# Kernel tuning notes

Hardware: AMD Instinct MI355X
Metric: run time of the kernel (lower is better)

## Reference

```python
import jax, jax.numpy as jnp
import numpy as np

B = 1024      # batch
DIN = 103     # generator/encoder input dim
L1, L2 = 64, 32   # encoder layer widths (latent = 32)
E = 8         # NUM_EXPERTS
GH = 64       # gating hidden width
H = 256       # generator hidden width
DOUT = 51     # generator output dim
EPS = 1e-5    # BatchNorm eps


def setup_inputs() -> dict:
    key = jax.random.key(0)
    ks = jax.random.split(key, 24)
    s = 0.05
    f32 = jnp.float32
    return {
        "x": jax.random.normal(ks[0], (B, DIN), f32),
        # encoder Linear + BN params
        "w1": jax.random.normal(ks[1], (L1, DIN), f32) * s,
        "b1": jnp.zeros((L1,), f32),
        "gamma1": jnp.ones((L1,), f32),
        "beta1": jnp.zeros((L1,), f32),
        "w2": jax.random.normal(ks[2], (L2, L1), f32) * s,
        "b2": jnp.zeros((L2,), f32),
        "gamma2": jnp.ones((L2,), f32),
        "beta2": jnp.zeros((L2,), f32),
        # gating MLP (latent 32 -> GH -> GH -> E, ELU, softmax)
        "gw1": jax.random.normal(ks[3], (GH, L2), f32) * s,
        "gb1": jnp.zeros((GH,), f32),
        "gw2": jax.random.normal(ks[4], (GH, GH), f32) * s,
        "gb2": jnp.zeros((GH,), f32),
        "gw3": jax.random.normal(ks[5], (E, GH), f32) * s,
        "gb3": jnp.zeros((E,), f32),
        # expert weight banks for 3-layer generator (MANN style)
        "ew1": jax.random.normal(ks[6], (E, DIN, H), f32) * s,
        "eb1": jnp.zeros((E, H), f32),
        "ew2": jax.random.normal(ks[7], (E, H, H), f32) * s,
        "eb2": jnp.zeros((E, H), f32),
        "ew3": jax.random.normal(ks[8], (E, H, DOUT), f32) * s,
        "eb3": jnp.zeros((E, DOUT), f32),
    }


def _batchnorm(h, gamma, beta):
    # training-mode BatchNorm1d: per-batch mean/var (biased var, matching torch)
    m = jnp.mean(h, axis=0)
    v = jnp.mean((h - m) ** 2, axis=0)
    return gamma * (h - m) * jax.lax.rsqrt(v + EPS) + beta


def reference(x, w1, b1, gamma1, beta1, w2, b2, gamma2, beta2,
              gw1, gb1, gw2, gb2, gw3, gb3,
              ew1, eb1, ew2, eb2, ew3, eb3):
    # in-place scale of last 3 features (x[:,100:103] *= 100)
    xs = x.at[:, 100:103].multiply(100.0)
    # encoder: Linear -> BN -> ReLU, twice
    h = jax.nn.relu(_batchnorm(xs @ w1.T + b1, gamma1, beta1))
    latent = jax.nn.relu(_batchnorm(h @ w2.T + b2, gamma2, beta2))
    # gating network -> blending coefficients BC [B, E]
    g = jax.nn.elu(latent @ gw1.T + gb1)
    g = jax.nn.elu(g @ gw2.T + gb2)
    bc = jax.nn.softmax(g @ gw3.T + gb3, axis=-1)
    # MANN-style generator: per-sample expert-blended weights
    wb1 = jnp.einsum('be,eih->bih', bc, ew1)   # [B, DIN, H]
    h1 = jax.nn.elu(jnp.einsum('bi,bih->bh', xs, wb1) + bc @ eb1)
    wb2 = jnp.einsum('be,ehk->bhk', bc, ew2)   # [B, H, H]
    h2 = jax.nn.elu(jnp.einsum('bh,bhk->bk', h1, wb2) + bc @ eb2)
    wb3 = jnp.einsum('be,eho->bho', bc, ew3)   # [B, H, DOUT]
    out = jnp.einsum('bh,bho->bo', h2, wb3) + bc @ eb3
    return out
```

## Files before the change

kernel.cpp:

```cpp
#include <hip/hip_runtime.h>
#include <math.h>


#define DIN 103
#define NE  8
#define HH  256
#define DOUT 51
#define EPSBN 1e-5f

typedef __attribute__((ext_vector_type(8))) short bf16x8;
typedef __attribute__((ext_vector_type(4))) float f32x4;
typedef __attribute__((ext_vector_type(8))) unsigned short us8;
typedef unsigned short ushort_t;

__device__ __forceinline__ float eluf(float v) { return v > 0.f ? v : (expf(v) - 1.f); }
__device__ __forceinline__ unsigned short bf16h(float f) {
  unsigned u = __float_as_uint(f);
  u += 0x7FFFu + ((u >> 16) & 1u);
  return (unsigned short)(u >> 16);
}
__device__ __forceinline__ float bf16f(unsigned short h) { return __uint_as_float(((unsigned)h) << 16); }
__device__ __forceinline__ void split_bf16(float v, unsigned short& h, unsigned short& l) {
  h = bf16h(v);
  l = bf16h(v - bf16f(h));
}
#define MFMA __builtin_amdgcn_mfma_f32_16x16x32_bf16

#define O_SLOTS1 0
#define O_SLOTS2 8192
#define O_BCG    12288
#define O_H1RAW  20480
#define O_H2RAW  86016
#define O_XSH    118784
#define O_XSL    184320
#define O_E1H    258048
#define O_E1L    389120
#define O_E2H    520192
#define O_E3H    782336
#define O_A1H    847872
#define O_A1L    978944
#define O_A2H    1110016
#define O_A2L    1241088

__global__ __launch_bounds__(256) void k_prep_enc1(
    const float* __restrict__ x, const float* __restrict__ w1, const float* __restrict__ b1,
    const float* __restrict__ ew1, const float* __restrict__ ew2, const float* __restrict__ ew3,
    float* __restrict__ ws) {
  __shared__ union {
    float tile[32][65];
    float xt[16][104];
    struct { float w1L[64 * DIN]; float xr[16][104]; float hb[16][64]; } e1;
  } sm;
  int bk = blockIdx.x, t = threadIdx.x;
  int l2 = t & 63, c = l2 & 15, q = l2 >> 4;

  if (bk < 256) {
    int nh = bk & 3, kc = (bk >> 2) & 7, e = bk >> 5;
    int k0 = kc * 32, n0 = nh * 64;
#pragma unroll
    for (int i = 0; i < 8; ++i) {
      int kl = (t >> 6) + i * 4;
      sm.tile[kl][t & 63] = ew2[((size_t)e * HH + k0 + kl) * HH + n0 + (t & 63)];
    }
    __syncthreads();
    int nsl = t >> 6;
    us8 H8;
#pragma unroll
    for (int j = 0; j < 8; ++j) H8[j] = bf16h(sm.tile[q * 8 + j][nsl * 16 + c]);
    size_t dst = (((size_t)(e * 16 + nh * 4 + nsl)) * 8 + kc) * 512 + l2 * 8;
    *(us8*)((ushort_t*)(ws + O_E2H) + dst) = H8;
  } else if (bk < 384) {
    int b2 = bk - 256;
    int nh = b2 & 3, kc = (b2 >> 2) & 3, e = b2 >> 4;
    int k0 = kc * 32, n0 = nh * 64;
#pragma unroll
    for (int i = 0; i < 8; ++i) {
      int kl = (t >> 6) + i * 4;
      int k = k0 + kl;
      sm.tile[kl][t & 63] = (k < DIN) ? ew1[((size_t)e * DIN + k) * HH + n0 + (t & 63)] : 0.f;
    }
    __syncthreads();
    int nsl = t >> 6;
    us8 H8, L8;
#pragma unroll
    for (int j = 0; j < 8; ++j) {
      unsigned short h, lo; split_bf16(sm.tile[q * 8 + j][nsl * 16 + c], h, lo);
      H8[j] = h; L8[j] = lo;
    }
    size_t dst = (((size_t)(e * 16 + nh * 4 + nsl)) * 4 + kc) * 512 + l2 * 8;
    *(us8*)((ushort_t*)(ws + O_E1H) + dst) = H8;
    *(us8*)((ushort_t*)(ws + O_E1L) + dst) = L8;
  } else if (bk < 448) {
    int b2 = bk - 384;
    int kc = b2 & 7, e = b2 >> 3;
    int k0 = kc * 32;
#pragma unroll
    for (int i = 0; i < 8; ++i) {
      int kl = (t >> 6) + i * 4;
      int n = t & 63;
      sm.tile[kl][n] = (n < DOUT) ? ew3[((size_t)e * HH + k0 + kl) * DOUT + n] : 0.f;
    }
    __syncthreads();
    int nsl = t >> 6;
    us8 H8;
#pragma unroll
    for (int j = 0; j < 8; ++j) H8[j] = bf16h(sm.tile[q * 8 + j][nsl * 16 + c]);
    size_t dst = (((size_t)(e * 4 + nsl)) * 8 + kc) * 512 + l2 * 8;
    *(us8*)((ushort_t*)(ws + O_E3H) + dst) = H8;
  } else if (bk < 512) {
    int msub = bk - 448;
    for (int i = t; i < 16 * 104; i += 256) {
      int b = i / 104, k = i - b * 104;
      float v = 0.f;
      if (k < DIN) { v = x[(size_t)(msub * 16 + b) * DIN + k]; if (k >= 100) v *= 100.f; }
      sm.xt[b][k] = v;
    }
    __syncthreads();
    int kc = t >> 6;
    int m = c;
    us8 H8, L8;
#pragma unroll
    for (int j = 0; j < 8; ++j) {
      int k = kc * 32 + q * 8 + j;
      float v = (k < 104) ? sm.xt[m][k] : 0.f;
      unsigned short h, lo; split_bf16(v, h, lo);
      H8[j] = h; L8[j] = lo;
    }
    size_t dst = ((size_t)msub * 4 + kc) * 512 + l2 * 8;
    *(us8*)((ushort_t*)(ws + O_XSH) + dst) = H8;
    *(us8*)((ushort_t*)(ws + O_XSL) + dst) = L8;
  } else {
    float* slots1 = ws + O_SLOTS1;
    float* h1raw  = ws + O_H1RAW;
    int bkl = bk - 512;
    int r0 = bkl * 16;
    for (int i = t; i < 64 * DIN; i += 256) sm.e1.w1L[i] = w1[i];
    for (int i = t; i < 16 * 104; i += 256) {
      int r = i / 104, c2 = i - r * 104;
      float v = 0.f;
      if (c2 < DIN) { v = x[(size_t)(r0 + r) * DIN + c2]; if (c2 >= 100) v *= 100.f; }
      sm.e1.xr[r][c2] = v;
    }
    __syncthreads();
#pragma unroll
    for (int i = 0; i < 4; ++i) {
      int idx = t + i * 256;
      int r = idx >> 6, j = idx & 63;
      float acc = b1[j];
      for (int k = 0; k < DIN; ++k) acc = fmaf(sm.e1.xr[r][k], sm.e1.w1L[j * DIN + k], acc);
      sm.e1.hb[r][j] = acc;
      h1raw[(size_t)(r0 + r) * 64 + j] = acc;
    }
    __syncthreads();
    if (t < 64) {
      float s = 0.f, qq = 0.f;
      for (int r = 0; r < 16; ++r) { float v = sm.e1.hb[r][t]; s += v; qq += v * v; }
      slots1[bkl * 128 + t] = s;
      slots1[bkl * 128 + 64 + t] = qq;
    }
  }
}

__global__ __launch_bounds__(256) void k_enc2(
    const float* __restrict__ gamma1, const float* __restrict__ beta1,
    const float* __restrict__ w2, const float* __restrict__ b2, float* __restrict__ ws) {
  __shared__ float w2T[64 * 33];
  __shared__ float red[128];
  __shared__ float sc1[64], sh1[64];
  __shared__ float h1b[16][64];
  __shared__ float hb2[16][32];
  float* slots1 = ws + O_SLOTS1;
  float* slots2 = ws + O_SLOTS2;
  float* h1raw  = ws + O_H1RAW;
  float* h2raw  = ws + O_H2RAW;
  int bk = blockIdx.x, t = threadIdx.x;
  int R0 = bk * 16;
  for (int i = t; i < 2048; i += 256) { int j = i >> 6, k = i & 63; w2T[k * 33 + j] = w2[i]; }
  if (t < 128) {
    float s = 0.f;
    for (int b = 0; b < 64; ++b) s += slots1[b * 128 + t];
    red[t] = s;
  }
  __syncthreads();
  if (t < 64) {
    float m = red[t] * (1.f / 1024.f);
    float v = red[64 + t] * (1.f / 1024.f) - m * m;
    float sc = gamma1[t] * rsqrtf(v + EPSBN);
    sc1[t] = sc; sh1[t] = beta1[t] - m * sc;
  }
  __syncthreads();
#pragma unroll
  for (int i = 0; i < 4; ++i) {
    int idx = t + i * 256;
    int r = idx >> 6, k = idx & 63;
    h1b[r][k] = fmaxf(fmaf(h1raw[(size_t)(R0 + r) * 64 + k], sc1[k], sh1[k]), 0.f);
  }
  __syncthreads();
#pragma unroll
  for (int i = 0; i < 2; ++i) {
    int o = t + i * 256;
    int r = o >> 5, j = o & 31;
    float acc = b2[j];
    for (int k = 0; k < 64; ++k) acc = fmaf(h1b[r][k], w2T[k * 33 + j], acc);
    hb2[r][j] = acc;
    h2raw[(size_t)(R0 + r) * 32 + j] = acc;
  }
  __syncthreads();
  if (t < 32) {
    float s = 0.f, q = 0.f;
    for (int r = 0; r < 16; ++r) { float v = hb2[r][t]; s += v; q += v * v; }
    slots2[bk * 64 + t] = s;
    slots2[bk * 64 + 32 + t] = q;
  }
}

__global__ __launch_bounds__(256) void k_gen1(
    const float* __restrict__ gamma2, const float* __restrict__ beta2,
    const float* __restrict__ gw1, const float* __restrict__ gb1,
    const float* __restrict__ gw2, const float* __restrict__ gb2,
    const float* __restrict__ gw3, const float* __restrict__ gb3,
    const float* __restrict__ eb1, float* __restrict__ ws) {
  __shared__ union {
    struct {
      float gw1L[64 * 33];
      float gw2L[64 * 65];
      float gw3L[8 * 65];
      float gb1L[64], gb2L[64], gb3L[8];
      float red2[64], sc2[32], sh2[32];
      float lat[16][32];
      float g1[16][64], g2[16][64];
    } gate;
    struct {
      float hT[64][17];
      float ebs[512];
    } comb;
  } U;
  __shared__ float bcL[16][8];

  const int blk = blockIdx.x, t = threadIdx.x;
  const int m = blk >> 2, g = blk & 3;
  const int wv = t >> 6, l = t & 63, c = l & 15, quad = l >> 4;
  const int R0 = m * 16;
  const float* slots2 = ws + O_SLOTS2;
  const float* h2raw  = ws + O_H2RAW;
  float* bcg = ws + O_BCG;
  const ushort_t* XsH = (const ushort_t*)(ws + O_XSH);
  const ushort_t* XsL = (const ushort_t*)(ws + O_XSL);
  const ushort_t* E1H = (const ushort_t*)(ws + O_E1H);
  const ushort_t* E1L = (const ushort_t*)(ws + O_E1L);

  bf16x8 a1h[4], a1l[4];
#pragma unroll
  for (int kc = 0; kc < 4; ++kc) {
    a1h[kc] = *(const bf16x8*)(XsH + ((size_t)m * 4 + kc) * 512 + l * 8);
    a1l[kc] = *(const bf16x8*)(XsL + ((size_t)m * 4 + kc) * 512 + l * 8);
  }

  for (int i = t; i < 2048; i += 256) { int j = i >> 5, k = i & 31; U.gate.gw1L[j * 33 + k] = gw1[i]; }
  for (int i = t; i < 4096; i += 256) { int j = i >> 6, k = i & 63; U.gate.gw2L[j * 65 + k] = gw2[i]; }
  for (int i = t; i < 512; i += 256) { int j = i >> 6, k = i & 63; U.gate.gw3L[j * 65 + k] = gw3[i]; }
  if (t < 64) { U.gate.gb1L[t] = gb1[t]; U.gate.gb2L[t] = gb2[t]; }
  if (t < 8) U.gate.gb3L[t] = gb3[t];
  if (t < 64) {
    float s = 0.f;
    for (int b = 0; b < 64; ++b) s += slots2[b * 64 + t];
    U.gate.red2[t] = s;
  }
  __syncthreads();
  if (t < 32) {
    float mm = U.gate.red2[t] * (1.f / 1024.f);
    float v = U.gate.red2[32 + t] * (1.f / 1024.f) - mm * mm;
    float sc = gamma2[t] * rsqrtf(v + EPSBN);
    U.gate.sc2[t] = sc; U.gate.sh2[t] = beta2[t] - mm * sc;
  }
  __syncthreads();
#pragma unroll
  for (int i = 0; i < 2; ++i) {
    int idx = t + i * 256;
    int r = idx >> 5, cc = idx & 31;
    U.gate.lat[r][cc] = fmaxf(fmaf(h2raw[(size_t)(R0 + r) * 32 + cc], U.gate.sc2[cc], U.gate.sh2[cc]), 0.f);
  }
  __syncthreads();
#pragma unroll
  for (int rr = 0; rr < 4; ++rr) {
    int r = wv * 4 + rr;
    float a1 = U.gate.gb1L[l];
    for (int k = 0; k < 32; ++k) a1 = fmaf(U.gate.gw1L[l * 33 + k], U.gate.lat[r][k], a1);
    U.gate.g1[r][l] = eluf(a1);
  }
  __syncthreads();
#pragma unroll
  for (int rr = 0; rr < 4; ++rr) {
    int r = wv * 4 + rr;
    float a2 = U.gate.gb2L[l];
    for (int k = 0; k < 64; ++k) a2 = fmaf(U.gate.gw2L[l * 65 + k], U.gate.g1[r][k], a2);
    U.gate.g2[r][l] = eluf(a2);
  }
  __syncthreads();
#pragma unroll
  for (int rr = 0; rr < 4; ++rr) {
    int r = wv * 4 + rr;
    if (l < 8) {
      float a3 = U.gate.gb3L[l];
      for (int k = 0; k < 64; ++k) a3 = fmaf(U.gate.gw3L[l * 65 + k], U.gate.g2[r][k], a3);
      float mx = a3;
      mx = fmaxf(mx, __shfl_xor(mx, 1));
      mx = fmaxf(mx, __shfl_xor(mx, 2));
      mx = fmaxf(mx, __shfl_xor(mx, 4));
      float p = expf(a3 - mx);
      float sp = p;
      sp += __shfl_xor(sp, 1); sp += __shfl_xor(sp, 2); sp += __shfl_xor(sp, 4);
      float bcv = p / sp;
      bcL[r][l] = bcv;
      if (g == 0) bcg[(size_t)(R0 + r) * 8 + l] = bcv;
    }
  }
  __syncthreads();

  for (int i = t; i < 512; i += 256) U.comb.ebs[i] = eb1[(i >> 6) * HH + g * 64 + (i & 63)];
  __syncthreads();
  const int ns = g * 4 + wv;
  f32x4 blend = {};
#pragma unroll
  for (int e = 0; e < NE; ++e) {
    float bcv[4];
#pragma unroll
    for (int r = 0; r < 4; ++r) bcv[r] = bcL[quad * 4 + r][e];
    f32x4 acc = {};
#pragma unroll
    for (int kc = 0; kc < 4; ++kc) {
      size_t bo = (((size_t)(e * 16 + ns)) * 4 + kc) * 512 + l * 8;
      bf16x8 bh = *(const bf16x8*)(E1H + bo);
      bf16x8 bl = *(const bf16x8*)(E1L + bo);
      acc = MFMA(a1h[kc], bh, acc, 0, 0, 0);
      acc = MFMA(a1l[kc], bh, acc, 0, 0, 0);
      acc = MFMA(a1h[kc], bl, acc, 0, 0, 0);
    }
    float ebv = U.comb.ebs[e * 64 + wv * 16 + c];
#pragma unroll
    for (int r = 0; r < 4; ++r) blend[r] = fmaf(bcv[r], acc[r] + ebv, blend[r]);
  }
#pragma unroll
  for (int r = 0; r < 4; ++r) U.comb.hT[wv * 16 + c][quad * 4 + r] = eluf(blend[r]);
  __syncthreads();
  if (t < 128) {
    int kcl = t >> 6, l2 = t & 63, row = l2 & 15, k0l = kcl * 32 + (l2 >> 4) * 8;
    us8 H, L;
#pragma unroll
    for (int j = 0; j < 8; ++j) {
      unsigned short h, lo; split_bf16(U.comb.hT[k0l + j][row], h, lo);
      H[j] = h; L[j] = lo;
    }
    size_t dst = ((size_t)m * 8 + g * 2 + kcl) * 512 + l2 * 8;
    *(us8*)((ushort_t*)(ws + O_A1H) + dst) = H;
    *(us8*)((ushort_t*)(ws + O_A1L) + dst) = L;
  }
}

__global__ __launch_bounds__(256) void k_gen2n(
    const float* __restrict__ eb2, float* __restrict__ ws) {
  __shared__ float hT[64][17];
  __shared__ float ebs[512];
  __shared__ float bcL[16][8];
  const int blk = blockIdx.x, t = threadIdx.x;
  const int m = blk >> 2, g = blk & 3;
  const int wv = t >> 6, l = t & 63, c = l & 15, quad = l >> 4;
  const int R0 = m * 16;
  const float* bcg = ws + O_BCG;
  const ushort_t* A1H = (const ushort_t*)(ws + O_A1H);
  const ushort_t* A1L = (const ushort_t*)(ws + O_A1L);
  const ushort_t* E2H = (const ushort_t*)(ws + O_E2H);

  if (t < 128) bcL[t >> 3][t & 7] = bcg[(size_t)(R0 + (t >> 3)) * 8 + (t & 7)];
  for (int i = t; i < 512; i += 256) ebs[i] = eb2[(i >> 6) * HH + g * 64 + (i & 63)];
  bf16x8 ah[8], al[8];
#pragma unroll
  for (int kc = 0; kc < 8; ++kc) {
    ah[kc] = *(const bf16x8*)(A1H + ((size_t)m * 8 + kc) * 512 + l * 8);
    al[kc] = *(const bf16x8*)(A1L + ((size_t)m * 8 + kc) * 512 + l * 8);
  }
  __syncthreads();
  const int ns = g * 4 + wv;
  f32x4 blend = {};
#pragma unroll
  for (int e = 0; e < NE; ++e) {
    float bcv[4];
#pragma unroll
    for (int r = 0; r < 4; ++r) bcv[r] = bcL[quad * 4 + r][e];
    f32x4 acc = {};
#pragma unroll
    for (int kc = 0; kc < 8; ++kc) {
      size_t bo = (((size_t)(e * 16 + ns)) * 8 + kc) * 512 + l * 8;
      bf16x8 bh = *(const bf16x8*)(E2H + bo);
      acc = MFMA(ah[kc], bh, acc, 0, 0, 0);
      acc = MFMA(al[kc], bh, acc, 0, 0, 0);
    }
    float ebv = ebs[e * 64 + wv * 16 + c];
#pragma unroll
    for (int r = 0; r < 4; ++r) blend[r] = fmaf(bcv[r], acc[r] + ebv, blend[r]);
  }
#pragma unroll
  for (int r = 0; r < 4; ++r) hT[wv * 16 + c][quad * 4 + r] = eluf(blend[r]);
  __syncthreads();
  if (t < 128) {
    int kcl = t >> 6, l2 = t & 63, row = l2 & 15, k0l = kcl * 32 + (l2 >> 4) * 8;
    us8 H, L;
#pragma unroll
    for (int j = 0; j < 8; ++j) {
      unsigned short h, lo; split_bf16(hT[k0l + j][row], h, lo);
      H[j] = h; L[j] = lo;
    }
    size_t dst = ((size_t)m * 8 + g * 2 + kcl) * 512 + l2 * 8;
    *(us8*)((ushort_t*)(ws + O_A2H) + dst) = H;
    *(us8*)((ushort_t*)(ws + O_A2L) + dst) = L;
  }
}

__global__ __launch_bounds__(512) void k_gen3(const float* __restrict__ eb3,
    const float* __restrict__ ws, float* __restrict__ out) {
  __shared__ float p3s[8][16][64];
  __shared__ float bcL[16][8];
  __shared__ float eb3L[8][64];
  const int bk = blockIdx.x, t = threadIdx.x;
  const int wv = t >> 6, l = t & 63, c = l & 15, quad = l >> 4;
  const int R0 = bk * 16;
  const float* bcg = ws + O_BCG;
  const ushort_t* A2H = (const ushort_t*)(ws + O_A2H);
  const ushort_t* A2L = (const ushort_t*)(ws + O_A2L);
  const ushort_t* E3H = (const ushort_t*)(ws + O_E3H);

  if (t < 128) bcL[t >> 3][t & 7] = bcg[(size_t)(R0 + (t >> 3)) * 8 + (t & 7)];
  { int e = t >> 6, n = t & 63; eb3L[e][n] = (n < DOUT) ? eb3[e * DOUT + n] : 0.f; }
  const int e = wv;
  f32x4 acc[4] = {};
#pragma unroll
  for (int kc = 0; kc < 8; ++kc) {
    bf16x8 ah = *(const bf16x8*)(A2H + ((size_t)bk * 8 + kc) * 512 + l * 8);
    bf16x8 al = *(const bf16x8*)(A2L + ((size_t)bk * 8 + kc) * 512 + l * 8);
#pragma unroll
    for (int nsi = 0; nsi < 4; ++nsi) {
      size_t bo = (((size_t)(e * 4 + nsi)) * 8 + kc) * 512 + l * 8;
      bf16x8 bh = *(const bf16x8*)(E3H + bo);
      acc[nsi] = MFMA(ah, bh, acc[nsi], 0, 0, 0);
      acc[nsi] = MFMA(al, bh, acc[nsi], 0, 0, 0);
    }
  }
#pragma unroll
  for (int nsi = 0; nsi < 4; ++nsi)
#pragma unroll
    for (int r = 0; r < 4; ++r)
      p3s[e][quad * 4 + r][nsi * 16 + c] = acc[nsi][r];
  __syncthreads();
#pragma unroll
  for (int i = 0; i < 2; ++i) {
    int idx = t + i * 512;
    int row = idx >> 6, col = idx & 63;
    float s = 0.f;
#pragma unroll
    for (int e2 = 0; e2 < 8; ++e2)
      s = fmaf(bcL[row][e2], p3s[e2][row][col] + eb3L[e2][col], s);
    if (col < DOUT) out[(size_t)(R0 + row) * DOUT + col] = s;
  }
}

extern "C" void kernel_launch(void* const* d_in, const int* in_sizes, int n_in,
                              void* d_out, int out_size, void* d_ws, size_t ws_size,
                              hipStream_t stream) {
  const float* x      = (const float*)d_in[0];
  const float* w1     = (const float*)d_in[1];
  const float* b1     = (const float*)d_in[2];
  const float* gamma1 = (const float*)d_in[3];
  const float* beta1  = (const float*)d_in[4];
  const float* w2     = (const float*)d_in[5];
  const float* b2     = (const float*)d_in[6];
  const float* gamma2 = (const float*)d_in[7];
  const float* beta2  = (const float*)d_in[8];
  const float* gw1    = (const float*)d_in[9];
  const float* gb1    = (const float*)d_in[10];
  const float* gw2    = (const float*)d_in[11];
  const float* gb2    = (const float*)d_in[12];
  const float* gw3    = (const float*)d_in[13];
  const float* gb3    = (const float*)d_in[14];
  const float* ew1    = (const float*)d_in[15];
  const float* eb1    = (const float*)d_in[16];
  const float* ew2    = (const float*)d_in[17];
  const float* eb2    = (const float*)d_in[18];
  const float* ew3    = (const float*)d_in[19];
  const float* eb3    = (const float*)d_in[20];
  float* wsf  = (float*)d_ws;
  float* outp = (float*)d_out;

  k_prep_enc1<<<576, 256, 0, stream>>>(x, w1, b1, ew1, ew2, ew3, wsf);
  k_enc2<<<64, 256, 0, stream>>>(gamma1, beta1, w2, b2, wsf);
  k_gen1<<<256, 256, 0, stream>>>(gamma2, beta2, gw1, gb1, gw2, gb2, gw3, gb3, eb1, wsf);
  k_gen2n<<<256, 256, 0, stream>>>(eb2, wsf);
  k_gen3<<<64, 512, 0, stream>>>(eb3, wsf, outp);
}
```

Baseline: 160.9 us.

## Fuse four post-prep kernels into one persistent kernel with grid barriers

Replaces the enc2, gen1, gen2 and gen3 launches with a single 256-block kernel. The stages are separated by software grid barriers built on an atomic counter in workspace, and that counter is reset by the prep kernel. The blend coefficients now stay in shared memory across stages instead of going through global memory, and gen3 runs on 64 of the blocks, each computing two experts per wave. This removes three kernel launch gaps. The cost is spin-wait barriers that depend on all 256 blocks being resident at once, and fewer blocks doing work in the final stage.

```diff
diff --git a/kernel.cpp b/kernel.cpp
--- a/kernel.cpp
+++ b/kernel.cpp
@@ -28,7 +28,6 @@
 
 #define O_SLOTS1 0
 #define O_SLOTS2 8192
-#define O_BCG    12288
 #define O_H1RAW  20480
 #define O_H2RAW  86016
 #define O_XSH    118784
@@ -41,6 +40,18 @@
 #define O_A1L    978944
 #define O_A2H    1110016
 #define O_A2L    1241088
+#define O_BAR    1372160
+
+__device__ __forceinline__ void gbar(unsigned* c) {
+  __syncthreads();
+  if (threadIdx.x == 0) {
+    __threadfence();
+    atomicAdd(c, 1u);
+    while (atomicAdd(c, 0u) < 256u) __builtin_amdgcn_s_sleep(2);
+    __threadfence();
+  }
+  __syncthreads();
+}
 
 __global__ __launch_bounds__(256) void k_prep_enc1(
     const float* __restrict__ x, const float* __restrict__ w1, const float* __restrict__ b1,
@@ -53,6 +64,7 @@
   } sm;
   int bk = blockIdx.x, t = threadIdx.x;
   int l2 = t & 63, c = l2 & 15, q = l2 >> 4;
+  if (bk == 0 && t < 4) ((unsigned*)(ws + O_BAR))[t] = 0u;
 
   if (bk < 256) {
     int nh = bk & 3, kc = (bk >> 2) & 7, e = bk >> 5;
@@ -161,79 +173,25 @@
   }
 }
 
-__global__ __launch_bounds__(256) void k_enc2(
+__global__ __launch_bounds__(256) void k_rest(
     const float* __restrict__ gamma1, const float* __restrict__ beta1,
-    const float* __restrict__ w2, const float* __restrict__ b2, float* __restrict__ ws) {
-  __shared__ float w2T[64 * 33];
-  __shared__ float red[128];
-  __shared__ float sc1[64], sh1[64];
-  __shared__ float h1b[16][64];
-  __shared__ float hb2[16][32];
-  float* slots1 = ws + O_SLOTS1;
-  float* slots2 = ws + O_SLOTS2;
-  float* h1raw  = ws + O_H1RAW;
-  float* h2raw  = ws + O_H2RAW;
-  int bk = blockIdx.x, t = threadIdx.x;
-  int R0 = bk * 16;
-  for (int i = t; i < 2048; i += 256) { int j = i >> 6, k = i & 63; w2T[k * 33 + j] = w2[i]; }
-  if (t < 128) {
-    float s = 0.f;
-    for (int b = 0; b < 64; ++b) s += slots1[b * 128 + t];
-    red[t] = s;
-  }
-  __syncthreads();
-  if (t < 64) {
-    float m = red[t] * (1.f / 1024.f);
-    float v = red[64 + t] * (1.f / 1024.f) - m * m;
-    float sc = gamma1[t] * rsqrtf(v + EPSBN);
-    sc1[t] = sc; sh1[t] = beta1[t] - m * sc;
-  }
-  __syncthreads();
-#pragma unroll
-  for (int i = 0; i < 4; ++i) {
-    int idx = t + i * 256;
-    int r = idx >> 6, k = idx & 63;
-    h1b[r][k] = fmaxf(fmaf(h1raw[(size_t)(R0 + r) * 64 + k], sc1[k], sh1[k]), 0.f);
-  }
-  __syncthreads();
-#pragma unroll
-  for (int i = 0; i < 2; ++i) {
-    int o = t + i * 256;
-    int r = o >> 5, j = o & 31;
-    float acc = b2[j];
-    for (int k = 0; k < 64; ++k) acc = fmaf(h1b[r][k], w2T[k * 33 + j], acc);
-    hb2[r][j] = acc;
-    h2raw[(size_t)(R0 + r) * 32 + j] = acc;
-  }
-  __syncthreads();
-  if (t < 32) {
-    float s = 0.f, q = 0.f;
-    for (int r = 0; r < 16; ++r) { float v = hb2[r][t]; s += v; q += v * v; }
-    slots2[bk * 64 + t] = s;
-    slots2[bk * 64 + 32 + t] = q;
-  }
-}
-
-__global__ __launch_bounds__(256) void k_gen1(
+    const float* __restrict__ w2, const float* __restrict__ b2,
     const float* __restrict__ gamma2, const float* __restrict__ beta2,
     const float* __restrict__ gw1, const float* __restrict__ gb1,
     const float* __restrict__ gw2, const float* __restrict__ gb2,
     const float* __restrict__ gw3, const float* __restrict__ gb3,
-    const float* __restrict__ eb1, float* __restrict__ ws) {
+    const float* __restrict__ eb1, const float* __restrict__ eb2,
+    const float* __restrict__ eb3,
+    float* __restrict__ ws, float* __restrict__ out) {
   __shared__ union {
-    struct {
-      float gw1L[64 * 33];
-      float gw2L[64 * 65];
-      float gw3L[8 * 65];
-      float gb1L[64], gb2L[64], gb3L[8];
-      float red2[64], sc2[32], sh2[32];
-      float lat[16][32];
-      float g1[16][64], g2[16][64];
-    } gate;
-    struct {
-      float hT[64][17];
-      float ebs[512];
-    } comb;
+    struct { float w2T[64 * 33]; float red[128]; float sc1[64], sh1[64];
+             float h1b[16][64]; float hb2[16][32]; } enc2;
+    struct { float gw1L[64 * 33]; float gw2L[64 * 65]; float gw3L[8 * 65];
+             float gb1L[64], gb2L[64], gb3L[8];
+             float red2[64], sc2[32], sh2[32];
+             float lat[16][32]; float g1[16][64], g2[16][64]; } gate;
+    struct { float hT[64][17]; float ebs[512]; } comb;
+    struct { float p3s[8][16][64]; float eb3L[8][64]; } g3;
   } U;
   __shared__ float bcL[16][8];
 
@@ -241,225 +199,261 @@
   const int m = blk >> 2, g = blk & 3;
   const int wv = t >> 6, l = t & 63, c = l & 15, quad = l >> 4;
   const int R0 = m * 16;
-  const float* slots2 = ws + O_SLOTS2;
-  const float* h2raw  = ws + O_H2RAW;
-  float* bcg = ws + O_BCG;
+  unsigned* bar = (unsigned*)(ws + O_BAR);
   const ushort_t* XsH = (const ushort_t*)(ws + O_XSH);
   const ushort_t* XsL = (const ushort_t*)(ws + O_XSL);
   const ushort_t* E1H = (const ushort_t*)(ws + O_E1H);
   const ushort_t* E1L = (const ushort_t*)(ws + O_E1L);
-
-  bf16x8 a1h[4], a1l[4];
-#pragma unroll
-  for (int kc = 0; kc < 4; ++kc) {
-    a1h[kc] = *(const bf16x8*)(XsH + ((size_t)m * 4 + kc) * 512 + l * 8);
-    a1l[kc] = *(const bf16x8*)(XsL + ((size_t)m * 4 + kc) * 512 + l * 8);
-  }
-
-  for (int i = t; i < 2048; i += 256) { int j = i >> 5, k = i & 31; U.gate.gw1L[j * 33 + k] = gw1[i]; }
-  for (int i = t; i < 4096; i += 256) { int j = i >> 6, k = i & 63; U.gate.gw2L[j * 65 + k] = gw2[i]; }
-  for (int i = t; i < 512; i += 256) { int j = i >> 6, k = i & 63; U.gate.gw3L[j * 65 + k] = gw3[i]; }
-  if (t < 64) { U.gate.gb1L[t] = gb1[t]; U.gate.gb2L[t] = gb2[t]; }
-  if (t < 8) U.gate.gb3L[t] = gb3[t];
-  if (t < 64) {
-    float s = 0.f;
-    for (int b = 0; b < 64; ++b) s += slots2[b * 64 + t];
-    U.gate.red2[t] = s;
-  }
-  __syncthreads();
-  if (t < 32) {
-    float mm = U.gate.red2[t] * (1.f / 1024.f);
-    float v = U.gate.red2[32 + t] * (1.f / 1024.f) - mm * mm;
-    float sc = gamma2[t] * rsqrtf(v + EPSBN);
-    U.gate.sc2[t] = sc; U.gate.sh2[t] = beta2[t] - mm * sc;
-  }
-  __syncthreads();
-#pragma unroll
-  for (int i = 0; i < 2; ++i) {
-    int idx = t + i * 256;
-    int r = idx >> 5, cc = idx & 31;
-    U.gate.lat[r][cc] = fmaxf(fmaf(h2raw[(size_t)(R0 + r) * 32 + cc], U.gate.sc2[cc], U.gate.sh2[cc]), 0.f);
-  }
-  __syncthreads();
-#pragma unroll
-  for (int rr = 0; rr < 4; ++rr) {
-    int r = wv * 4 + rr;
-    float a1 = U.gate.gb1L[l];
-    for (int k = 0; k < 32; ++k) a1 = fmaf(U.gate.gw1L[l * 33 + k], U.gate.lat[r][k], a1);
-    U.gate.g1[r][l] = eluf(a1);
-  }
-  __syncthreads();
-#pragma unroll
-  for (int rr = 0; rr < 4; ++rr) {
-    int r = wv * 4 + rr;
-    float a2 = U.gate.gb2L[l];
-    for (int k = 0; k < 64; ++k) a2 = fmaf(U.gate.gw2L[l * 65 + k], U.gate.g1[r][k], a2);
-    U.gate.g2[r][l] = eluf(a2);
-  }
-  __syncthreads();
-#pragma unroll
-  for (int rr = 0; rr < 4; ++rr) {
-    int r = wv * 4 + rr;
-    if (l < 8) {
-      float a3 = U.gate.gb3L[l];
-      for (int k = 0; k < 64; ++k) a3 = fmaf(U.gate.gw3L[l * 65 + k], U.gate.g2[r][k], a3);
-      float mx = a3;
-      mx = fmaxf(mx, __shfl_xor(mx, 1));
-      mx = fmaxf(mx, __shfl_xor(mx, 2));
-      mx = fmaxf(mx, __shfl_xor(mx, 4));
-      float p = expf(a3 - mx);
-      float sp = p;
-      sp += __shfl_xor(sp, 1); sp += __shfl_xor(sp, 2); sp += __shfl_xor(sp, 4);
-      float bcv = p / sp;
-      bcL[r][l] = bcv;
-      if (g == 0) bcg[(size_t)(R0 + r) * 8 + l] = bcv;
-    }
-  }
-  __syncthreads();
-
-  for (int i = t; i < 512; i += 256) U.comb.ebs[i] = eb1[(i >> 6) * HH + g * 64 + (i & 63)];
-  __syncthreads();
-  const int ns = g * 4 + wv;
-  f32x4 blend = {};
-#pragma unroll
-  for (int e = 0; e < NE; ++e) {
-    float bcv[4];
-#pragma unroll
-    for (int r = 0; r < 4; ++r) bcv[r] = bcL[quad * 4 + r][e];
-    f32x4 acc = {};
+  const ushort_t* E2H = (const ushort_t*)(ws + O_E2H);
+  const ushort_t* E3H = (const ushort_t*)(ws + O_E3H);
+
+  if (blk < 64) {
+    float* slots1 = ws + O_SLOTS1;
+    float* slots2 = ws + O_SLOTS2;
+    float* h1raw  = ws + O_H1RAW;
+    float* h2raw  = ws + O_H2RAW;
+    const int R0e = blk * 16;
+    for (int i = t; i < 2048; i += 256) { int j = i >> 6, k = i & 63; U.enc2.w2T[k * 33 + j] = w2[i]; }
+    if (t < 128) {
+      float s = 0.f;
+      for (int b = 0; b < 64; ++b) s += slots1[b * 128 + t];
+      U.enc2.red[t] = s;
+    }
+    __syncthreads();
+    if (t < 64) {
+      float mm = U.enc2.red[t] * (1.f / 1024.f);
+      float v = U.enc2.red[64 + t] * (1.f / 1024.f) - mm * mm;
+      float sc = gamma1[t] * rsqrtf(v + EPSBN);
+      U.enc2.sc1[t] = sc; U.enc2.sh1[t] = beta1[t] - mm * sc;
+    }
+    __syncthreads();
+#pragma unroll
+    for (int i = 0; i < 4; ++i) {
+      int idx = t + i * 256;
+      int r = idx >> 6, k = idx & 63;
+      U.enc2.h1b[r][k] = fmaxf(fmaf(h1raw[(size_t)(R0e + r) * 64 + k], U.enc2.sc1[k], U.enc2.sh1[k]), 0.f);
+    }
+    __syncthreads();
+#pragma unroll
+    for (int i = 0; i < 2; ++i) {
+      int o = t + i * 256;
+      int r = o >> 5, j = o & 31;
+      float acc = b2[j];
+      for (int k = 0; k < 64; ++k) acc = fmaf(U.enc2.h1b[r][k], U.enc2.w2T[k * 33 + j], acc);
+      U.enc2.hb2[r][j] = acc;
+      h2raw[(size_t)(R0e + r) * 32 + j] = acc;
+    }
+    __syncthreads();
+    if (t < 32) {
+      float s = 0.f, q = 0.f;
+      for (int r = 0; r < 16; ++r) { float v = U.enc2.hb2[r][t]; s += v; q += v * v; }
+      slots2[blk * 64 + t] = s;
+      slots2[blk * 64 + 32 + t] = q;
+    }
+  }
+  gbar(bar + 0);
+
+  {
+    const float* slots2 = ws + O_SLOTS2;
+    const float* h2raw  = ws + O_H2RAW;
+    bf16x8 a1h[4], a1l[4];
 #pragma unroll
     for (int kc = 0; kc < 4; ++kc) {
-      size_t bo = (((size_t)(e * 16 + ns)) * 4 + kc) * 512 + l * 8;
-      bf16x8 bh = *(const bf16x8*)(E1H + bo);
-      bf16x8 bl = *(const bf16x8*)(E1L + bo);
-      acc = MFMA(a1h[kc], bh, acc, 0, 0, 0);
-      acc = MFMA(a1l[kc], bh, acc, 0, 0, 0);
-      acc = MFMA(a1h[kc], bl, acc, 0, 0, 0);
-    }
-    float ebv = U.comb.ebs[e * 64 + wv * 16 + c];
-#pragma unroll
-    for (int r = 0; r < 4; ++r) blend[r] = fmaf(bcv[r], acc[r] + ebv, blend[r]);
-  }
-#pragma unroll
-  for (int r = 0; r < 4; ++r) U.comb.hT[wv * 16 + c][quad * 4 + r] = eluf(blend[r]);
-  __syncthreads();
-  if (t < 128) {
-    int kcl = t >> 6, l2 = t & 63, row = l2 & 15, k0l = kcl * 32 + (l2 >> 4) * 8;
-    us8 H, L;
-#pragma unroll
-    for (int j = 0; j < 8; ++j) {
-      unsigned short h, lo; split_bf16(U.comb.hT[k0l + j][row], h, lo);
-      H[j] = h; L[j] = lo;
-    }
-    size_t dst = ((size_t)m * 8 + g * 2 + kcl) * 512 + l2 * 8;
-    *(us8*)((ushort_t*)(ws + O_A1H) + dst) = H;
-    *(us8*)((ushort_t*)(ws + O_A1L) + dst) = L;
-  }
-}
-
-__global__ __launch_bounds__(256) void k_gen2n(
-    const float* __restrict__ eb2, float* __restrict__ ws) {
-  __shared__ float hT[64][17];
-  __shared__ float ebs[512];
-  __shared__ float bcL[16][8];
-  const int blk = blockIdx.x, t = threadIdx.x;
-  const int m = blk >> 2, g = blk & 3;
-  const int wv = t >> 6, l = t & 63, c = l & 15, quad = l >> 4;
-  const int R0 = m * 16;
-  const float* bcg = ws + O_BCG;
-  const ushort_t* A1H = (const ushort_t*)(ws + O_A1H);
-  const ushort_t* A1L = (const ushort_t*)(ws + O_A1L);
-  const ushort_t* E2H = (const ushort_t*)(ws + O_E2H);
-
-  if (t < 128) bcL[t >> 3][t & 7] = bcg[(size_t)(R0 + (t >> 3)) * 8 + (t & 7)];
-  for (int i = t; i < 512; i += 256) ebs[i] = eb2[(i >> 6) * HH + g * 64 + (i & 63)];
-  bf16x8 ah[8], al[8];
-#pragma unroll
-  for (int kc = 0; kc < 8; ++kc) {
-    ah[kc] = *(const bf16x8*)(A1H + ((size_t)m * 8 + kc) * 512 + l * 8);
-    al[kc] = *(const bf16x8*)(A1L + ((size_t)m * 8 + kc) * 512 + l * 8);
-  }
-  __syncthreads();
-  const int ns = g * 4 + wv;
-  f32x4 blend = {};
-#pragma unroll
-  for (int e = 0; e < NE; ++e) {
-    float bcv[4];
-#pragma unroll
-    for (int r = 0; r < 4; ++r) bcv[r] = bcL[quad * 4 + r][e];
-    f32x4 acc = {};
+      a1h[kc] = *(const bf16x8*)(XsH + ((size_t)m * 4 + kc) * 512 + l * 8);
+      a1l[kc] = *(const bf16x8*)(XsL + ((size_t)m * 4 + kc) * 512 + l * 8);
+    }
+    for (int i = t; i < 2048; i += 256) { int j = i >> 5, k = i & 31; U.gate.gw1L[j * 33 + k] = gw1[i]; }
+    for (int i = t; i < 4096; i += 256) { int j = i >> 6, k = i & 63; U.gate.gw2L[j * 65 + k] = gw2[i]; }
+    for (int i = t; i < 512; i += 256) { int j = i >> 6, k = i & 63; U.gate.gw3L[j * 65 + k] = gw3[i]; }
+    if (t < 64) { U.gate.gb1L[t] = gb1[t]; U.gate.gb2L[t] = gb2[t]; }
+    if (t < 8) U.gate.gb3L[t] = gb3[t];
+    if (t < 64) {
+      float s = 0.f;
+      for (int b = 0; b < 64; ++b) s += slots2[b * 64 + t];
+      U.gate.red2[t] = s;
+    }
+    __syncthreads();
+    if (t < 32) {
+      float mm = U.gate.red2[t] * (1.f / 1024.f);
+      float v = U.gate.red2[32 + t] * (1.f / 1024.f) - mm * mm;
+      float sc = gamma2[t] * rsqrtf(v + EPSBN);
+      U.gate.sc2[t] = sc; U.gate.sh2[t] = beta2[t] - mm * sc;
+    }
+    __syncthreads();
+#pragma unroll
+    for (int i = 0; i < 2; ++i) {
+      int idx = t + i * 256;
+      int r = idx >> 5, cc = idx & 31;
+      U.gate.lat[r][cc] = fmaxf(fmaf(h2raw[(size_t)(R0 + r) * 32 + cc], U.gate.sc2[cc], U.gate.sh2[cc]), 0.f);
+    }
+    __syncthreads();
+#pragma unroll
+    for (int rr = 0; rr < 4; ++rr) {
+      int r = wv * 4 + rr;
+      float a1 = U.gate.gb1L[l];
+      for (int k = 0; k < 32; ++k) a1 = fmaf(U.gate.gw1L[l * 33 + k], U.gate.lat[r][k], a1);
+      U.gate.g1[r][l] = eluf(a1);
+    }
+    __syncthreads();
+#pragma unroll
+    for (int rr = 0; rr < 4; ++rr) {
+      int r = wv * 4 + rr;
+      float a2 = U.gate.gb2L[l];
+      for (int k = 0; k < 64; ++k) a2 = fmaf(U.gate.gw2L[l * 65 + k], U.gate.g1[r][k], a2);
+      U.gate.g2[r][l] = eluf(a2);
+    }
+    __syncthreads();
+#pragma unroll
+    for (int rr = 0; rr < 4; ++rr) {
+      int r = wv * 4 + rr;
+      if (l < 8) {
+        float a3 = U.gate.gb3L[l];
+        for (int k = 0; k < 64; ++k) a3 = fmaf(U.gate.gw3L[l * 65 + k], U.gate.g2[r][k], a3);
+        float mx = a3;
+        mx = fmaxf(mx, __shfl_xor(mx, 1));
+        mx = fmaxf(mx, __shfl_xor(mx, 2));
+        mx = fmaxf(mx, __shfl_xor(mx, 4));
+        float p = expf(a3 - mx);
+        float sp = p;
+        sp += __shfl_xor(sp, 1); sp += __shfl_xor(sp, 2); sp += __shfl_xor(sp, 4);
+        bcL[r][l] = p / sp;
+      }
+    }
+    __syncthreads();
+
+    for (int i = t; i < 512; i += 256) U.comb.ebs[i] = eb1[(i >> 6) * HH + g * 64 + (i & 63)];
+    __syncthreads();
+    const int ns = g * 4 + wv;
+    f32x4 blend = {};
+#pragma unroll
+    for (int e = 0; e < NE; ++e) {
+      float bcv[4];
+#pragma unroll
+      for (int r = 0; r < 4; ++r) bcv[r] = bcL[quad * 4 + r][e];
+      f32x4 acc = {};
+#pragma unroll
+      for (int kc = 0; kc < 4; ++kc) {
+        size_t bo = (((size_t)(e * 16 + ns)) * 4 + kc) * 512 + l * 8;
+        bf16x8 bh = *(const bf16x8*)(E1H + bo);
+        bf16x8 bl = *(const bf16x8*)(E1L + bo);
+        acc = MFMA(a1h[kc], bh, acc, 0, 0, 0);
+        acc = MFMA(a1l[kc], bh, acc, 0, 0, 0);
+        acc = MFMA(a1h[kc], bl, acc, 0, 0, 0);
+      }
+      float ebv = U.comb.ebs[e * 64 + wv * 16 + c];
+#pragma unroll
+      for (int r = 0; r < 4; ++r) blend[r] = fmaf(bcv[r], acc[r] + ebv, blend[r]);
+    }
+#pragma unroll
+    for (int r = 0; r < 4; ++r) U.comb.hT[wv * 16 + c][quad * 4 + r] = eluf(blend[r]);
+    __syncthreads();
+    if (t < 128) {
+      int kcl = t >> 6, l2 = t & 63, row = l2 & 15, k0l = kcl * 32 + (l2 >> 4) * 8;
+      us8 H, L;
+#pragma unroll
+      for (int j = 0; j < 8; ++j) {
+        unsigned short h, lo; split_bf16(U.comb.hT[k0l + j][row], h, lo);
+        H[j] = h; L[j] = lo;
+      }
+      size_t dst = ((size_t)m * 8 + g * 2 + kcl) * 512 + l2 * 8;
+      *(us8*)((ushort_t*)(ws + O_A1H) + dst) = H;
+      *(us8*)((ushort_t*)(ws + O_A1L) + dst) = L;
+    }
+  }
+  gbar(bar + 1);
+
+  {
+    const ushort_t* A1H = (const ushort_t*)(ws + O_A1H);
+    const ushort_t* A1L = (const ushort_t*)(ws + O_A1L);
+    for (int i = t; i < 512; i += 256) U.comb.ebs[i] = eb2[(i >> 6) * HH + g * 64 + (i & 63)];
+    bf16x8 ah[8], al[8];
 #pragma unroll
     for (int kc = 0; kc < 8; ++kc) {
-      size_t bo = (((size_t)(e * 16 + ns)) * 8 + kc) * 512 + l * 8;
-      bf16x8 bh = *(const bf16x8*)(E2H + bo);
-      acc = MFMA(ah[kc], bh, acc, 0, 0, 0);
-      acc = MFMA(al[kc], bh, acc, 0, 0, 0);
-    }
-    float ebv = ebs[e * 64 + wv * 16 + c];
-#pragma unroll
-    for (int r = 0; r < 4; ++r) blend[r] = fmaf(bcv[r], acc[r] + ebv, blend[r]);
-  }
-#pragma unroll
-  for (int r = 0; r < 4; ++r) hT[wv * 16 + c][quad * 4 + r] = eluf(blend[r]);
-  __syncthreads();
-  if (t < 128) {
-    int kcl = t >> 6, l2 = t & 63, row = l2 & 15, k0l = kcl * 32 + (l2 >> 4) * 8;
-    us8 H, L;
-#pragma unroll
-    for (int j = 0; j < 8; ++j) {
-      unsigned short h, lo; split_bf16(hT[k0l + j][row], h, lo);
-      H[j] = h; L[j] = lo;
-    }
-    size_t dst = ((size_t)m * 8 + g * 2 + kcl) * 512 + l2 * 8;
-    *(us8*)((ushort_t*)(ws + O_A2H) + dst) = H;
-    *(us8*)((ushort_t*)(ws + O_A2L) + dst) = L;
-  }
-}
-
-__global__ __launch_bounds__(512) void k_gen3(const float* __restrict__ eb3,
-    const float* __restrict__ ws, float* __restrict__ out) {
-  __shared__ float p3s[8][16][64];
-  __shared__ float bcL[16][8];
-  __shared__ float eb3L[8][64];
-  const int bk = blockIdx.x, t = threadIdx.x;
-  const int wv = t >> 6, l = t & 63, c = l & 15, quad = l >> 4;
-  const int R0 = bk * 16;
-  const float* bcg = ws + O_BCG;
-  const ushort_t* A2H = (const ushort_t*)(ws + O_A2H);
-  const ushort_t* A2L = (const ushort_t*)(ws + O_A2L);
-  const ushort_t* E3H = (const ushort_t*)(ws + O_E3H);
-
-  if (t < 128) bcL[t >> 3][t & 7] = bcg[(size_t)(R0 + (t >> 3)) * 8 + (t & 7)];
-  { int e = t >> 6, n = t & 63; eb3L[e][n] = (n < DOUT) ? eb3[e * DOUT + n] : 0.f; }
-  const int e = wv;
-  f32x4 acc[4] = {};
-#pragma unroll
-  for (int kc = 0; kc < 8; ++kc) {
-    bf16x8 ah = *(const bf16x8*)(A2H + ((size_t)bk * 8 + kc) * 512 + l * 8);
-    bf16x8 al = *(const bf16x8*)(A2L + ((size_t)bk * 8 + kc) * 512 + l * 8);
-#pragma unroll
-    for (int nsi = 0; nsi < 4; ++nsi) {
-      size_t bo = (((size_t)(e * 4 + nsi)) * 8 + kc) * 512 + l * 8;
-      bf16x8 bh = *(const bf16x8*)(E3H + bo);
-      acc[nsi] = MFMA(ah, bh, acc[nsi], 0, 0, 0);
-      acc[nsi] = MFMA(al, bh, acc[nsi], 0, 0, 0);
-    }
-  }
-#pragma unroll
-  for (int nsi = 0; nsi < 4; ++nsi)
-#pragma unroll
-    for (int r = 0; r < 4; ++r)
-      p3s[e][quad * 4 + r][nsi * 16 + c] = acc[nsi][r];
-  __syncthreads();
-#pragma unroll
-  for (int i = 0; i < 2; ++i) {
-    int idx = t + i * 512;
-    int row = idx >> 6, col = idx & 63;
-    float s = 0.f;
-#pragma unroll
-    for (int e2 = 0; e2 < 8; ++e2)
-      s = fmaf(bcL[row][e2], p3s[e2][row][col] + eb3L[e2][col], s);
-    if (col < DOUT) out[(size_t)(R0 + row) * DOUT + col] = s;
+      ah[kc] = *(const bf16x8*)(A1H + ((size_t)m * 8 + kc) * 512 + l * 8);
+      al[kc] = *(const bf16x8*)(A1L + ((size_t)m * 8 + kc) * 512 + l * 8);
+    }
+    __syncthreads();
+    const int ns = g * 4 + wv;
+    f32x4 blend = {};
+#pragma unroll
+    for (int e = 0; e < NE; ++e) {
+      float bcv[4];
+#pragma unroll
+      for (int r = 0; r < 4; ++r) bcv[r] = bcL[quad * 4 + r][e];
+      f32x4 acc = {};
+#pragma unroll
+      for (int kc = 0; kc < 8; ++kc) {
+        size_t bo = (((size_t)(e * 16 + ns)) * 8 + kc) * 512 + l * 8;
+        bf16x8 bh = *(const bf16x8*)(E2H + bo);
+        acc = MFMA(ah[kc], bh, acc, 0, 0, 0);
+        acc = MFMA(al[kc], bh, acc, 0, 0, 0);
+      }
+      float ebv = U.comb.ebs[e * 64 + wv * 16 + c];
+#pragma unroll
+      for (int r = 0; r < 4; ++r) blend[r] = fmaf(bcv[r], acc[r] + ebv, blend[r]);
+    }
+#pragma unroll
+    for (int r = 0; r < 4; ++r) U.comb.hT[wv * 16 + c][quad * 4 + r] = eluf(blend[r]);
+    __syncthreads();
+    if (t < 128) {
+      int kcl = t >> 6, l2 = t & 63, row = l2 & 15, k0l = kcl * 32 + (l2 >> 4) * 8;
+      us8 H, L;
+#pragma unroll
+      for (int j = 0; j < 8; ++j) {
+        unsigned short h, lo; split_bf16(U.comb.hT[k0l + j][row], h, lo);
+        H[j] = h; L[j] = lo;
+      }
+      size_t dst = ((size_t)m * 8 + g * 2 + kcl) * 512 + l2 * 8;
+      *(us8*)((ushort_t*)(ws + O_A2H) + dst) = H;
+      *(us8*)((ushort_t*)(ws + O_A2L) + dst) = L;
+    }
+  }
+  gbar(bar + 2);
+
+  if (g == 0) {
+    const ushort_t* A2H = (const ushort_t*)(ws + O_A2H);
+    const ushort_t* A2L = (const ushort_t*)(ws + O_A2L);
+    for (int i = t; i < 512; i += 256) {
+      int e2 = i >> 6, n = i & 63;
+      U.g3.eb3L[e2][n] = (n < DOUT) ? eb3[e2 * DOUT + n] : 0.f;
+    }
+    bf16x8 ah[8], al[8];
+#pragma unroll
+    for (int kc = 0; kc < 8; ++kc) {
+      ah[kc] = *(const bf16x8*)(A2H + ((size_t)m * 8 + kc) * 512 + l * 8);
+      al[kc] = *(const bf16x8*)(A2L + ((size_t)m * 8 + kc) * 512 + l * 8);
+    }
+#pragma unroll
+    for (int ee = 0; ee < 2; ++ee) {
+      const int e = wv + ee * 4;
+      f32x4 acc[4] = {};
+#pragma unroll
+      for (int kc = 0; kc < 8; ++kc) {
+#pragma unroll
+        for (int nsi = 0; nsi < 4; ++nsi) {
+          size_t bo = (((size_t)(e * 4 + nsi)) * 8 + kc) * 512 + l * 8;
+          bf16x8 bh = *(const bf16x8*)(E3H + bo);
+          acc[nsi] = MFMA(ah[kc], bh, acc[nsi], 0, 0, 0);
+          acc[nsi] = MFMA(al[kc], bh, acc[nsi], 0, 0, 0);
+        }
+      }
+#pragma unroll
+      for (int nsi = 0; nsi < 4; ++nsi)
+#pragma unroll
+        for (int r = 0; r < 4; ++r)
+          U.g3.p3s[e][quad * 4 + r][nsi * 16 + c] = acc[nsi][r];
+    }
+    __syncthreads();
+#pragma unroll
+    for (int i = 0; i < 4; ++i) {
+      int idx = t + i * 256;
+      int row = idx >> 6, col = idx & 63;
+      float s = 0.f;
+#pragma unroll
+      for (int e2 = 0; e2 < 8; ++e2)
+        s = fmaf(bcL[row][e2], U.g3.p3s[e2][row][col] + U.g3.eb3L[e2][col], s);
+      if (col < DOUT) out[(size_t)(R0 + row) * DOUT + col] = s;
+    }
   }
 }
 
@@ -491,8 +485,7 @@
   float* outp = (float*)d_out;
 
   k_prep_enc1<<<576, 256, 0, stream>>>(x, w1, b1, ew1, ew2, ew3, wsf);
-  k_enc2<<<64, 256, 0, stream>>>(gamma1, beta1, w2, b2, wsf);
-  k_gen1<<<256, 256, 0, stream>>>(gamma2, beta2, gw1, gb1, gw2, gb2, gw3, gb3, eb1, wsf);
-  k_gen2n<<<256, 256, 0, stream>>>(eb2, wsf);
-  k_gen3<<<64, 512, 0, stream>>>(eb3, wsf, outp);
-}
+  k_rest<<<256, 256, 0, stream>>>(gamma1, beta1, w2, b2, gamma2, beta2,
+                                  gw1, gb1, gw2, gb2, gw3, gb3,
+                                  eb1, eb2, eb3, wsf, outp);
+}
```

Measured after the change: 198.8 us. 23.6% more time.
